# Kernel tuning notes

Hardware: AMD Instinct MI355X
Metric: run time of the kernel (lower is better)

## Reference

```python
import jax, jax.numpy as jnp
import numpy as np

N, E, B, F_IN, C, K = 200000, 3200000, 128, 128, 10, 30
D_CAT = 97  # 32+32+32+1 concatenated GCN outputs


def setup_inputs() -> dict:
    key = jax.random.key(0)
    ks = jax.random.split(key, 12)
    s = 0.1
    return {
        "x": jax.random.normal(ks[0], (N, F_IN), jnp.float32),
        "edge_index": jax.random.randint(ks[1], (2, E), 0, N, jnp.int32),
        "batch": jnp.sort(jax.random.randint(ks[2], (N,), 0, B, jnp.int32)),
        "W1": jax.random.normal(ks[3], (F_IN, 32), jnp.float32) * s,
        "b1": jnp.zeros((32,), jnp.float32),
        "W2": jax.random.normal(ks[4], (32, 32), jnp.float32) * s,
        "b2": jnp.zeros((32,), jnp.float32),
        "W3": jax.random.normal(ks[5], (32, 32), jnp.float32) * s,
        "b3": jnp.zeros((32,), jnp.float32),
        "W4": jax.random.normal(ks[6], (32, 1), jnp.float32) * s,
        "b4": jnp.zeros((1,), jnp.float32),
        "conv5_w": jax.random.normal(ks[7], (16, 1, 97), jnp.float32) * s,
        "conv5_b": jnp.zeros((16,), jnp.float32),
        "conv6_w": jax.random.normal(ks[8], (32, 16, 5), jnp.float32) * s,
        "conv6_b": jnp.zeros((32,), jnp.float32),
        "fc1_w": jax.random.normal(ks[9], (352, 128), jnp.float32) * s,
        "fc1_b": jnp.zeros((128,), jnp.float32),
        "fc2_w": jax.random.normal(ks[10], (128, C), jnp.float32) * s,
        "fc2_b": jnp.zeros((C,), jnp.float32),
    }


def _gcn(x, W, b, src, dst, enorm, self_norm):
    # PyG GCNConv: h = xW; out = sum_j norm_ij * h_j (incl. self loop) + b
    h = x @ W
    agg = jax.ops.segment_sum(h[src] * enorm[:, None], dst, num_segments=h.shape[0])
    return agg + h * self_norm[:, None] + b


def _conv1d(x, w, b, stride):
    y = jax.lax.conv_general_dilated(x, w, (stride,), 'VALID',
                                     dimension_numbers=('NCH', 'OIH', 'NCH'))
    return y + b[None, :, None]


def reference(x, edge_index, batch, W1, b1, W2, b2, W3, b3, W4, b4,
              conv5_w, conv5_b, conv6_w, conv6_b, fc1_w, fc1_b, fc2_w, fc2_b):
    src, dst = edge_index[0], edge_index[1]
    # remove_self_loops (zero edge weight) then GCN adds self loop of weight 1
    w = (src != dst).astype(x.dtype)
    deg = jax.ops.segment_sum(w, dst, num_segments=N) + 1.0
    dinv = jax.lax.rsqrt(deg)
    enorm = w * dinv[src] * dinv[dst]   # per-edge sym norm
    self_norm = 1.0 / deg               # self-loop norm = dinv[i]^2

    x1 = jnp.tanh(_gcn(x, W1, b1, src, dst, enorm, self_norm))
    x2 = jnp.tanh(_gcn(x1, W2, b2, src, dst, enorm, self_norm))
    x3 = jnp.tanh(_gcn(x2, W3, b3, src, dst, enorm, self_norm))
    x4 = jnp.tanh(_gcn(x3, W4, b4, src, dst, enorm, self_norm))
    xc = jnp.concatenate([x1, x2, x3, x4], axis=-1)  # [N, 97]

    # SortAggregation(k=30): per-graph top-k nodes by last channel (descending)
    keyf = xc[:, -1]
    graph_ids = jnp.arange(B, dtype=batch.dtype)
    scores = jnp.where(batch[None, :] == graph_ids[:, None], keyf[None, :],
                       jnp.float32(-jnp.inf))         # [B, N]
    topv, topi = jax.lax.top_k(scores, K)              # [B, K]
    feats = xc[topi]                                   # [B, K, 97]
    feats = jnp.where(jnp.isfinite(topv)[..., None], feats, 0.0)  # pad rows -> 0
    z = feats.reshape(B, 1, K * D_CAT)                 # [B, 1, 2910]

    z = jax.nn.relu(_conv1d(z, conv5_w, conv5_b, 97))  # [B, 16, 30]
    z = jax.lax.reduce_window(z, -jnp.inf, jax.lax.max,
                              (1, 1, 2), (1, 1, 2), 'VALID')  # [B, 16, 15]
    z = jax.nn.relu(_conv1d(z, conv6_w, conv6_b, 1))   # [B, 32, 11]
    z = z.reshape(B, -1)                               # [B, 352]
    h = jax.nn.relu(z @ fc1_w + fc1_b)                 # dropout = identity (eval)
    return jax.nn.log_softmax(h @ fc2_w + fc2_b, axis=-1)
```

## Files before the change

### kernel.cpp

```cpp
#include <hip/hip_runtime.h>
#include <math.h>

#define TPB 256
#define TOPK 30
#define NGRAPH 128
#define TKCAP 4096
#define BSHIFT 11
#define NBMAX 128
#define FSHIFT 8
#define NFMAX 800
#define FCAP 4608


__global__ void bhist(const int* __restrict__ src, const int* __restrict__ dst,
                      int* __restrict__ btot, int E) {
    __shared__ int bcnt[NBMAX];
    int t = threadIdx.x;
    int base = blockIdx.x * 2048;
    int lim = E - base; if (lim > 2048) lim = 2048;
    for (int i = t; i < NBMAX; i += 256) bcnt[i] = 0;
    __syncthreads();
    for (int i = t; i < lim; i += 256) {
        int s = src[base + i], d = dst[base + i];
        if (s != d) atomicAdd(&bcnt[d >> BSHIFT], 1);
    }
    __syncthreads();
    for (int i = t; i < NBMAX; i += 256)
        if (bcnt[i] > 0) atomicAdd(&btot[i], bcnt[i]);
}

__global__ void bucket_scan(const int* __restrict__ btot, int* __restrict__ bbase,
                            int nbuckets) {
    __shared__ int ls[NBMAX];
    int t = threadIdx.x;
    int v = (t < nbuckets) ? btot[t] : 0;
    ls[t] = v;
    __syncthreads();
    for (int o = 1; o < NBMAX; o <<= 1) {
        int x = 0;
        if (t >= o) x = ls[t - o];
        __syncthreads();
        ls[t] += x;
        __syncthreads();
    }
    if (t < nbuckets) bbase[t] = ls[t] - v;
}

__global__ void bin_edges(const int* __restrict__ src, const int* __restrict__ dst,
                          const int* __restrict__ bbase_g, int* __restrict__ gcur,
                          int2* __restrict__ scratch, int E) {
    __shared__ int2 eds[2048];
    __shared__ int bcnt[NBMAX], bbase[NBMAX], boff[NBMAX];
    int t = threadIdx.x;
    int base = blockIdx.x * 2048;
    int lim = E - base; if (lim > 2048) lim = 2048;
    for (int i = t; i < NBMAX; i += 256) { bcnt[i] = 0; boff[i] = 0; }
    __syncthreads();
    for (int i = t; i < lim; i += 256) {
        int s = src[base + i], d = dst[base + i];
        if (s == d) d = -1;
        eds[i] = make_int2(s, d);
        if (d >= 0) atomicAdd(&bcnt[d >> BSHIFT], 1);
    }
    __syncthreads();
    for (int i = t; i < NBMAX; i += 256) {
        if (bcnt[i] > 0)
            bbase[i] = bbase_g[i] + atomicAdd(&gcur[i], bcnt[i]);
    }
    __syncthreads();
    for (int i = t; i < lim; i += 256) {
        int2 ed = eds[i];
        if (ed.y >= 0) {
            int b = ed.y >> BSHIFT;
            int pos = bbase[b] + atomicAdd(&boff[b], 1);
            scratch[pos] = ed;
        }
    }
}

__global__ void bucket_count(const int2* __restrict__ scratch,
                             const int* __restrict__ bbase, const int* __restrict__ btot,
                             int* __restrict__ rowptr, float* __restrict__ dinv,
                             float* __restrict__ snorm, int N, int NB) {
    __shared__ int hist[1 << BSHIFT];
    __shared__ int ls2[256];
    int b = blockIdx.x, t = threadIdx.x;
    int nlo = b << BSHIFT;
    int nn = N - nlo; if (nn > (1 << BSHIFT)) nn = 1 << BSHIFT;
    for (int i = t; i < (1 << BSHIFT); i += 256) hist[i] = 0;
    __syncthreads();
    int lo = bbase[b], hi = lo + btot[b];
    for (int e = lo + t; e < hi; e += 256)
        atomicAdd(&hist[scratch[e].y - nlo], 1);
    __syncthreads();
    int loc[8]; int run = 0;
    #pragma unroll
    for (int j = 0; j < 8; ++j) { loc[j] = run; run += hist[t * 8 + j]; }
    ls2[t] = run;
    __syncthreads();
    for (int o = 1; o < 256; o <<= 1) {
        int x = (t >= o) ? ls2[t - o] : 0;
        __syncthreads();
        ls2[t] += x;
        __syncthreads();
    }
    int base = bbase[b] + ls2[t] - run;
    #pragma unroll
    for (int j = 0; j < 8; ++j) {
        int i = t * 8 + j;
        if (i < nn) {
            rowptr[nlo + i] = base + loc[j];
            int c = hist[i];
            float deg = (float)c + 1.0f;
            dinv[nlo + i] = 1.0f / sqrtf(deg);
            snorm[nlo + i] = 1.0f / deg;
        }
    }
    if (b == NB - 1 && t == 0) rowptr[N] = bbase[b] + btot[b];
}

__global__ void bin2(const int2* __restrict__ scratch, const int* __restrict__ rowptr,
                     int* __restrict__ fcur, int2* __restrict__ scratch2, int N, int E) {
    __shared__ int fcnt[NFMAX], fbase[NFMAX], foff[NFMAX];
    int t = threadIdx.x;
    int En = rowptr[N];
    int base = blockIdx.x * 8192;
    if (base >= En) return;
    int lim = En - base; if (lim > 8192) lim = 8192;
    for (int i = t; i < NFMAX; i += 256) { fcnt[i] = 0; foff[i] = 0; }
    __syncthreads();
    for (int i = t; i < lim; i += 256) {
        int d = scratch[base + i].y;
        atomicAdd(&fcnt[d >> FSHIFT], 1);
    }
    __syncthreads();
    for (int fi = t; fi < NFMAX; fi += 256) {
        if (fcnt[fi] > 0)
            fbase[fi] = rowptr[fi << FSHIFT] + atomicAdd(&fcur[fi], fcnt[fi]);
    }
    __syncthreads();
    for (int i = t; i < lim; i += 256) {
        int2 ed = scratch[base + i];
        int fi = ed.y >> FSHIFT;
        int pos = fbase[fi] + atomicAdd(&foff[fi], 1);
        scratch2[pos] = ed;
    }
}

__global__ __launch_bounds__(256) void scatter_sort(const int2* __restrict__ scratch2,
                                                    const int* __restrict__ rowptr,
                                                    const float* __restrict__ dinv,
                                                    int2* __restrict__ eprec, int N) {
    __shared__ int srcA[FCAP], dstA[FCAP], inv[FCAP];
    __shared__ int hist[1 << FSHIFT];
    __shared__ int hcur[1 << FSHIFT];
    int f = blockIdx.x, t = threadIdx.x;
    int nlo = f << FSHIFT;
    int nhi = nlo + (1 << FSHIFT); if (nhi > N) nhi = N;
    int lo = rowptr[nlo], hi = rowptr[nhi];
    int span = hi - lo;
    for (int i = t; i < (1 << FSHIFT); i += 256) hist[i] = 0;
    __syncthreads();
    if (span <= FCAP) {
        for (int i = t; i < span; i += 256) {
            int2 ed = scratch2[lo + i];
            srcA[i] = ed.x; dstA[i] = ed.y;
            atomicAdd(&hist[ed.y - nlo], 1);
        }
        __syncthreads();
        int v = hist[t];
        hcur[t] = v;
        __syncthreads();
        for (int o = 1; o < 256; o <<= 1) {
            int x = (t >= o) ? hcur[t - o] : 0;
            __syncthreads();
            hcur[t] += x;
            __syncthreads();
        }
        int excl = hcur[t] - v;
        __syncthreads();
        hcur[t] = excl;
        __syncthreads();
        for (int i = t; i < span; i += 256) {
            int slot = atomicAdd(&hcur[dstA[i] - nlo], 1);
            inv[slot] = i;
        }
        __syncthreads();
        for (int p = t; p < span; p += 256) {
            int i = inv[p];
            int s = srcA[i], d = dstA[i];
            eprec[lo + p] = make_int2(s, __float_as_int(dinv[s] * dinv[d]));
        }
    } else {
        for (int e = lo + t; e < hi; e += 256) {
            int2 ed = scratch2[e];
            int d = ed.y;
            int p = rowptr[d] + atomicAdd(&hist[d - nlo], 1);
            eprec[p] = make_int2(ed.x, __float_as_int(dinv[ed.x] * dinv[d]));
        }
    }
}


__global__ void mm_128_32(const float* __restrict__ X, const float* __restrict__ W,
                          float* __restrict__ H, int n) {
    __shared__ float Ws[128 * 32];
    __shared__ float xs[32 * 128];
    int t = threadIdx.x;
    int rbase = blockIdx.x * 32;
    #pragma unroll
    for (int j = 0; j < 4; ++j) {
        int idx = t + 256 * j;
        *(float4*)(Ws + idx * 4) = *(const float4*)(W + idx * 4);
        int row = rbase + (idx >> 5);
        float4 v = make_float4(0.f, 0.f, 0.f, 0.f);
        if (row < n) v = *(const float4*)(X + (long)rbase * 128 + idx * 4);
        *(float4*)(xs + idx * 4) = v;
    }
    __syncthreads();
    int c4 = (t & 7) * 4, r = t >> 3;
    int row = rbase + r;
    if (row >= n) return;
    float ac0 = 0.f, ac1 = 0.f, ac2 = 0.f, ac3 = 0.f;
    #pragma unroll 8
    for (int k0 = 0; k0 < 128; k0 += 4) {
        float4 xv = *(const float4*)(xs + r * 128 + k0);
        #pragma unroll
        for (int j = 0; j < 4; ++j) {
            float xj = (j == 0) ? xv.x : (j == 1) ? xv.y : (j == 2) ? xv.z : xv.w;
            float4 wv = *(const float4*)(Ws + (k0 + j) * 32 + c4);
            ac0 += xj * wv.x; ac1 += xj * wv.y; ac2 += xj * wv.z; ac3 += xj * wv.w;
        }
    }
    *(float4*)(H + (long)row * 32 + c4) = make_float4(ac0, ac1, ac2, ac3);
}

__global__ void mm_32_32(const float* __restrict__ X, const float* __restrict__ W,
                         float* __restrict__ H, int n) {
    __shared__ float Ws[32 * 32];
    __shared__ float xs[32 * 32];
    int t = threadIdx.x;
    int rbase = blockIdx.x * 32;
    {
        *(float4*)(Ws + t * 4) = *(const float4*)(W + t * 4);
        int row = rbase + (t >> 3);
        float4 v = make_float4(0.f, 0.f, 0.f, 0.f);
        if (row < n) v = *(const float4*)(X + (long)rbase * 32 + t * 4);
        *(float4*)(xs + t * 4) = v;
    }
    __syncthreads();
    int c4 = (t & 7) * 4, r = t >> 3;
    int row = rbase + r;
    if (row >= n) return;
    float ac0 = 0.f, ac1 = 0.f, ac2 = 0.f, ac3 = 0.f;
    #pragma unroll
    for (int k0 = 0; k0 < 32; k0 += 4) {
        float4 xv = *(const float4*)(xs + r * 32 + k0);
        #pragma unroll
        for (int j = 0; j < 4; ++j) {
            float xj = (j == 0) ? xv.x : (j == 1) ? xv.y : (j == 2) ? xv.z : xv.w;
            float4 wv = *(const float4*)(Ws + (k0 + j) * 32 + c4);
            ac0 += xj * wv.x; ac1 += xj * wv.y; ac2 += xj * wv.z; ac3 += xj * wv.w;
        }
    }
    *(float4*)(H + (long)row * 32 + c4) = make_float4(ac0, ac1, ac2, ac3);
}

__global__ void mm_32_1(const float* __restrict__ X, const float* __restrict__ W,
                        float* __restrict__ H4, int n) {
    int gid = blockIdx.x * blockDim.x + threadIdx.x;
    int node = gid >> 3, l = gid & 7;
    if (node >= n) return;
    float4 v = *(const float4*)(X + (long)node * 32 + l * 4);
    float s = v.x * W[l * 4] + v.y * W[l * 4 + 1] + v.z * W[l * 4 + 2] + v.w * W[l * 4 + 3];
    s += __shfl_xor(s, 1, 64);
    s += __shfl_xor(s, 2, 64);
    s += __shfl_xor(s, 4, 64);
    if (l == 0) H4[node] = s;
}


__global__ void agg32(const float* __restrict__ H, const int2* __restrict__ eprec,
                      const int* __restrict__ rowptr,
                      const float* __restrict__ snorm, const float* __restrict__ bias,
                      float* __restrict__ OUT, int n) {
    int gid = blockIdx.x * blockDim.x + threadIdx.x;
    int node = gid >> 3, l = gid & 7;
    if (node >= n) return;
    int beg = rowptr[node], end = rowptr[node + 1];
    float ax = 0.f, ay = 0.f, az = 0.f, aw = 0.f;
    int e0 = beg;
    for (; e0 + 8 <= end; e0 += 8) {
        int2 ed = eprec[e0 + l];
        int ss[8]; float ww[8];
        #pragma unroll
        for (int j = 0; j < 8; ++j) {
            ss[j] = __shfl(ed.x, j, 8);
            ww[j] = __shfl(__int_as_float(ed.y), j, 8);
        }
        float4 hv[8];
        #pragma unroll
        for (int j = 0; j < 8; ++j)
            hv[j] = *(const float4*)(H + (long)ss[j] * 32 + l * 4);
        #pragma unroll
        for (int j = 0; j < 8; ++j) {
            ax += hv[j].x * ww[j]; ay += hv[j].y * ww[j];
            az += hv[j].z * ww[j]; aw += hv[j].w * ww[j];
        }
    }
    if (e0 < end) {
        int m = end - e0;
        int2 ed = (l < m) ? eprec[e0 + l] : make_int2(0, 0);
        for (int j = 0; j < m; ++j) {
            int s = __shfl(ed.x, j, 8);
            float w = __shfl(__int_as_float(ed.y), j, 8);
            float4 hv = *(const float4*)(H + (long)s * 32 + l * 4);
            ax += hv.x * w; ay += hv.y * w; az += hv.z * w; aw += hv.w * w;
        }
    }
    float sn = snorm[node];
    float4 hv = *(const float4*)(H + (long)node * 32 + l * 4);
    float4 bv = *(const float4*)(bias + l * 4);
    float4 o;
    o.x = tanhf(ax + hv.x * sn + bv.x);
    o.y = tanhf(ay + hv.y * sn + bv.y);
    o.z = tanhf(az + hv.z * sn + bv.z);
    o.w = tanhf(aw + hv.w * sn + bv.w);
    *(float4*)(OUT + (long)node * 32 + l * 4) = o;
}

__global__ void agg1(const float* __restrict__ H4, const int2* __restrict__ eprec,
                     const int* __restrict__ rowptr,
                     const float* __restrict__ snorm, const float* __restrict__ b4,
                     float* __restrict__ X4, int n) {
    int node = blockIdx.x * blockDim.x + threadIdx.x;
    if (node >= n) return;
    int beg = rowptr[node], end = rowptr[node + 1];
    float acc = 0.f;
    for (int e = beg; e < end; ++e) {
        int2 ed = eprec[e];
        acc += H4[ed.x] * __int_as_float(ed.y);
    }
    X4[node] = tanhf(acc + H4[node] * snorm[node] + b4[0]);
}


__global__ void graph_start(const int* __restrict__ batch, int* __restrict__ gstart,
                            int n, int B) {
    int i = blockIdx.x * blockDim.x + threadIdx.x;
    if (i >= n) return;
    int b = batch[i];
    int bp = (i == 0) ? -1 : batch[i - 1];
    for (int g = bp + 1; g <= b; ++g) gstart[g] = i;
    if (i == n - 1) {
        for (int g = b + 1; g <= B; ++g) gstart[g] = n;
    }
}


__global__ __launch_bounds__(512) void topk_head(
        const float* __restrict__ x1, const float* __restrict__ x2,
        const float* __restrict__ x3, const float* __restrict__ x4,
        const int* __restrict__ gstart,
        const float* __restrict__ w5, const float* __restrict__ b5,
        const float* __restrict__ w6, const float* __restrict__ b6,
        const float* __restrict__ fw1, const float* __restrict__ fb1,
        const float* __restrict__ fw2, const float* __restrict__ fb2,
        float* __restrict__ out) {
    int g = blockIdx.x;
    int t = threadIdx.x;
    __shared__ int topi_l[TOPK];
    __shared__ int selg[TOPK];
    __shared__ float lv[4 * TOPK];
    __shared__ int li[4 * TOPK];
    __shared__ float vals[TKCAP];
    __shared__ float wbv[8];
    __shared__ int wbi[8];
    __shared__ float ws5[16 * 97];
    __shared__ float ws6[32 * 16 * 5];
    __shared__ float wf2[128 * 10];
    __shared__ float part[4][128];
    __shared__ float feats[TOPK][97];
    __shared__ float c5[16][30];
    __shared__ float p6[16][15];
    __shared__ float z[352];
    __shared__ float hh[128];
    __shared__ float oo[10];

    int beg = gstart[g], end = gstart[g + 1];
    int range = end - beg;

    if (range <= 2048) {
        if (t >= 256) {
            int u = t - 256;
            for (int i = u; i < 16 * 97; i += 256) ws5[i] = w5[i];
            for (int i = u; i < 32 * 16 * 5; i += 256) ws6[i] = w6[i];
            for (int i = u; i < 128 * 10; i += 256) wf2[i] = fw2[i];
        } else {
            int wv = t >> 6, l = t & 63;
            int chunk = (range + 3) >> 2;
            int cbeg = wv * chunk;
            int cend = cbeg + chunk; if (cend > range) cend = range;
            float rv[8];
            #pragma unroll
            for (int j = 0; j < 8; ++j) {
                int i = cbeg + l + (j << 6);
                rv[j] = (i < cend) ? x4[beg + i] : -INFINITY;
            }
            for (int k = 0; k < TOPK; ++k) {
                float best = -INFINITY;
                int bj = -1;
                #pragma unroll
                for (int j = 0; j < 8; ++j)
                    if (rv[j] > best) { best = rv[j]; bj = j; }
                int bi = (bj < 0) ? 0x7fffffff : cbeg + (bj << 6) + l;
                #pragma unroll
                for (int off = 1; off < 64; off <<= 1) {
                    float ov = __shfl_xor(best, off, 64);
                    int oi = __shfl_xor(bi, off, 64);
                    if (ov > best || (ov == best && oi < bi)) { best = ov; bi = oi; }
                }
                if (l == 0) { lv[wv * TOPK + k] = best; li[wv * TOPK + k] = bi; }
                if (bi != 0x7fffffff && ((bi - cbeg) & 63) == l) {
                    int wj = (bi - cbeg) >> 6;
                    #pragma unroll
                    for (int j = 0; j < 8; ++j)
                        if (j == wj) rv[j] = -INFINITY;
                }
            }
        }
        __syncthreads();
        if (t < 64) {
            float mv0 = lv[t];
            int   mi0 = li[t];
            int i1 = t + 64;
            float mv1 = (i1 < 120) ? lv[i1] : -INFINITY;
            int   mi1 = (i1 < 120) ? li[i1] : 0x7fffffff;
            for (int k = 0; k < TOPK; ++k) {
                float best = mv0; int bi = mi0;
                if (mv1 > best || (mv1 == best && mi1 < bi)) { best = mv1; bi = mi1; }
                #pragma unroll
                for (int off = 1; off < 64; off <<= 1) {
                    float ov = __shfl_xor(best, off, 64);
                    int oi = __shfl_xor(bi, off, 64);
                    if (ov > best || (ov == best && oi < bi)) { best = ov; bi = oi; }
                }
                if (t == 0)
                    topi_l[k] = (bi == 0x7fffffff) ? -1 : beg + bi;
                if (mi0 == bi) mv0 = -INFINITY;
                if (mi1 == bi) mv1 = -INFINITY;
            }
        }
    } else {
        if (t >= 256) {
            int u = t - 256;
            for (int i = u; i < 16 * 97; i += 256) ws5[i] = w5[i];
            for (int i = u; i < 32 * 16 * 5; i += 256) ws6[i] = w6[i];
            for (int i = u; i < 128 * 10; i += 256) wf2[i] = fw2[i];
        }
        int lim = range < TKCAP ? range : TKCAP;
        for (int i = t; i < lim; i += 512) vals[i] = x4[beg + i];
        __syncthreads();
        for (int k = 0; k < TOPK; ++k) {
            float best = -INFINITY;
            int bi = 0x7fffffff;
            for (int i = t; i < lim; i += 512) {
                float v = vals[i];
                if (v > best) { best = v; bi = i; }
            }
            for (int i = TKCAP + t; i < range; i += 512) {
                int gi = beg + i;
                bool taken = false;
                for (int j = 0; j < k; ++j)
                    if (selg[j] == gi) { taken = true; break; }
                if (taken) continue;
                float v = x4[gi];
                if (v > best || (v == best && i < bi)) { best = v; bi = i; }
            }
            #pragma unroll
            for (int off = 1; off < 64; off <<= 1) {
                float ov = __shfl_xor(best, off, 64);
                int oi = __shfl_xor(bi, off, 64);
                if (ov > best || (ov == best && oi < bi)) { best = ov; bi = oi; }
            }
            if ((t & 63) == 0) { wbv[t >> 6] = best; wbi[t >> 6] = bi; }
            __syncthreads();
            if (t == 0) {
                float bv = wbv[0]; int bi0 = wbi[0];
                for (int wq = 1; wq < 8; ++wq)
                    if (wbv[wq] > bv || (wbv[wq] == bv && wbi[wq] < bi0)) { bv = wbv[wq]; bi0 = wbi[wq]; }
                int gl = (bi0 == 0x7fffffff) ? -1 : beg + bi0;
                selg[k] = gl;
                topi_l[k] = gl;
                if (bi0 != 0x7fffffff && bi0 < TKCAP) vals[bi0] = -INFINITY;
            }
            __syncthreads();
        }
    }
    __syncthreads();

    for (int idx = t; idx < TOPK * 97; idx += 512) {
        int k = idx / 97, j = idx % 97;
        int node = topi_l[k];
        float v = 0.f;
        if (node >= 0) {
            if (j < 32) v = x1[(long)node * 32 + j];
            else if (j < 64) v = x2[(long)node * 32 + (j - 32)];
            else if (j < 96) v = x3[(long)node * 32 + (j - 64)];
            else v = x4[node];
        }
        feats[k][j] = v;
    }
    __syncthreads();

    for (int idx = t; idx < 16 * 30; idx += 512) {
        int oc = idx / 30, k = idx % 30;
        float acc = b5[oc];
        for (int j = 0; j < 97; ++j) acc += ws5[oc * 97 + j] * feats[k][j];
        c5[oc][k] = fmaxf(acc, 0.f);
    }
    __syncthreads();

    for (int idx = t; idx < 16 * 15; idx += 512) {
        int oc = idx / 15, k = idx % 15;
        p6[oc][k] = fmaxf(c5[oc][2 * k], c5[oc][2 * k + 1]);
    }
    __syncthreads();

    for (int idx = t; idx < 32 * 11; idx += 512) {
        int oc = idx / 11, tt = idx % 11;
        float acc = b6[oc];
        for (int ic = 0; ic < 16; ++ic)
            for (int j = 0; j < 5; ++j)
                acc += ws6[(oc * 16 + ic) * 5 + j] * p6[ic][tt + j];
        z[idx] = fmaxf(acc, 0.f);
    }
    __syncthreads();

    {
        int o = t & 127, s = t >> 7;
        float acc = 0.f;
        int i0 = s * 88, i1 = i0 + 88;
        for (int i = i0; i < i1; ++i) acc += z[i] * fw1[i * 128 + o];
        part[s][o] = acc;
    }
    __syncthreads();
    if (t < 128) {
        float v = fb1[t] + ((part[0][t] + part[1][t]) + (part[2][t] + part[3][t]));
        hh[t] = fmaxf(v, 0.f);
    }
    __syncthreads();

    if (t < 10) {
        float acc = fb2[t];
        for (int j = 0; j < 128; ++j) acc += hh[j] * wf2[j * 10 + t];
        oo[t] = acc;
    }
    __syncthreads();

    if (t < 10) {
        float m = -INFINITY;
        for (int c = 0; c < 10; ++c) m = fmaxf(m, oo[c]);
        float s = 0.f;
        for (int c = 0; c < 10; ++c) s += expf(oo[c] - m);
        out[g * 10 + t] = oo[t] - m - logf(s);
    }
}


extern "C" void kernel_launch(void* const* d_in, const int* in_sizes, int n_in,
                              void* d_out, int out_size, void* d_ws, size_t ws_size,
                              hipStream_t stream) {
    const float* x     = (const float*)d_in[0];
    const int*   ei    = (const int*)d_in[1];
    const int*   batch = (const int*)d_in[2];
    const float* W1 = (const float*)d_in[3];
    const float* b1 = (const float*)d_in[4];
    const float* W2 = (const float*)d_in[5];
    const float* b2 = (const float*)d_in[6];
    const float* W3 = (const float*)d_in[7];
    const float* b3 = (const float*)d_in[8];
    const float* W4 = (const float*)d_in[9];
    const float* b4 = (const float*)d_in[10];
    const float* w5 = (const float*)d_in[11];
    const float* b5 = (const float*)d_in[12];
    const float* w6 = (const float*)d_in[13];
    const float* b6 = (const float*)d_in[14];
    const float* fw1 = (const float*)d_in[15];
    const float* fb1 = (const float*)d_in[16];
    const float* fw2 = (const float*)d_in[17];
    const float* fb2 = (const float*)d_in[18];

    const int N = in_sizes[0] / 128;
    const int E = in_sizes[1] / 2;
    const int* src = ei;
    const int* dst = ei + E;

    char* w = (char*)d_ws;
    size_t off = 0;
    auto alloc = [&](size_t bytes) -> void* {
        void* p = w + off;
        off = (off + bytes + 255) & ~(size_t)255;
        return p;
    };

    int*   gcur   = (int*)alloc(NBMAX * 4);
    int*   btot   = (int*)alloc(NBMAX * 4);
    int*   fcur   = (int*)alloc(NFMAX * 4);
    int*   bbase  = (int*)alloc(NBMAX * 4);
    int*   gstart = (int*)alloc((size_t)(NGRAPH + 1) * 4);
    int*   rowptr = (int*)alloc((size_t)(N + 1) * 4);
    float* dinv   = (float*)alloc((size_t)N * 4);
    float* snorm  = (float*)alloc((size_t)N * 4);
    int2*  eprec  = (int2*)alloc((size_t)E * 8);
    float* hbuf   = (float*)alloc((size_t)N * 32 * 4);
    float* x1     = (float*)alloc((size_t)N * 32 * 4);
    float* x2     = (float*)alloc((size_t)N * 32 * 4);
    float* x3     = (float*)alloc((size_t)N * 32 * 4);
    float* h4     = (float*)alloc((size_t)N * 4);
    float* x4     = (float*)alloc((size_t)N * 4);

    int2* scratch  = (int2*)hbuf;
    int2* scratch2 = (int2*)x1;

    hipMemsetAsync(gcur, 0, (size_t)(2 * NBMAX + NFMAX) * 4, stream);

    const int NB = (N + (1 << BSHIFT) - 1) >> BSHIFT;
    const int NF = (N + (1 << FSHIFT) - 1) >> FSHIFT;
    const int EB = (E + 2047) / 2048;

    graph_start<<<(N + TPB - 1) / TPB, TPB, 0, stream>>>(batch, gstart, N, NGRAPH);
    bhist<<<EB, TPB, 0, stream>>>(src, dst, btot, E);
    bucket_scan<<<1, NBMAX, 0, stream>>>(btot, bbase, NB);
    bin_edges<<<EB, TPB, 0, stream>>>(src, dst, bbase, gcur, scratch, E);
    bucket_count<<<NB, TPB, 0, stream>>>(scratch, bbase, btot, rowptr, dinv, snorm, N, NB);
    bin2<<<(E + 8191) / 8192, TPB, 0, stream>>>(scratch, rowptr, fcur, scratch2, N, E);
    scatter_sort<<<NF, 256, 0, stream>>>(scratch2, rowptr, dinv, eprec, N);

    mm_128_32<<<(N + 31) / 32, 256, 0, stream>>>(x, W1, hbuf, N);
    agg32<<<((size_t)N * 8 + TPB - 1) / TPB, TPB, 0, stream>>>(hbuf, eprec, rowptr,
                                                               snorm, b1, x1, N);
    mm_32_32<<<(N + 31) / 32, 256, 0, stream>>>(x1, W2, hbuf, N);
    agg32<<<((size_t)N * 8 + TPB - 1) / TPB, TPB, 0, stream>>>(hbuf, eprec, rowptr,
                                                               snorm, b2, x2, N);
    mm_32_32<<<(N + 31) / 32, 256, 0, stream>>>(x2, W3, hbuf, N);
    agg32<<<((size_t)N * 8 + TPB - 1) / TPB, TPB, 0, stream>>>(hbuf, eprec, rowptr,
                                                               snorm, b3, x3, N);
    mm_32_1<<<((size_t)N * 8 + TPB - 1) / TPB, TPB, 0, stream>>>(x3, W4, h4, N);
    agg1<<<(N + TPB - 1) / TPB, TPB, 0, stream>>>(h4, eprec, rowptr, snorm, b4, x4, N);

    topk_head<<<NGRAPH, 512, 0, stream>>>(x1, x2, x3, x4, gstart,
                                          w5, b5, w6, b6, fw1, fb1, fw2, fb2,
                                          (float*)d_out);
}
```

Baseline: 554.5 us.

## Replace iterative top-k selection with per-wave bitonic sort and sorted merge

In the small-graph path of the top-k head kernel, all 8 waves now each load up to 256 keys and bitonic-sort them in registers with shuffles. Each wave writes its top 30, and a single wave then bitonic-sorts the 240 candidates to get the final top-k. This replaces 30 rounds of argmax-plus-shuffle reductions in 4 waves followed by a 30-round merge. Weight loading moves to the remaining 448 threads after the per-wave sort. The fixed bitonic network costs more shuffle steps per wave but has no serial loop over k, and it assumes each wave's chunk fits in 256 elements (range at most 2048).

```diff
diff --git a/kernel.cpp b/kernel.cpp
--- a/kernel.cpp
+++ b/kernel.cpp
@@ -358,6 +358,43 @@
 }
 
 
+#define GTP(av,ai,bv,bi) (((av) > (bv)) || ((av) == (bv) && (ai) < (bi)))
+
+__device__ __forceinline__ void bsort256(float& v0, float& v1, float& v2, float& v3,
+                                         int& i0, int& i1, int& i2, int& i3, int lane) {
+    for (int k = 2; k <= 256; k <<= 1) {
+        for (int j = k >> 1; j > 0; j >>= 1) {
+            if (j == 64) {
+                { bool down = ((lane) & k) == 0;
+                  bool agt = GTP(v0, i0, v1, i1);
+                  if (down != agt) { float tv = v0; v0 = v1; v1 = tv; int ti = i0; i0 = i1; i1 = ti; } }
+                { bool down = ((lane + 128) & k) == 0;
+                  bool agt = GTP(v2, i2, v3, i3);
+                  if (down != agt) { float tv = v2; v2 = v3; v3 = tv; int ti = i2; i2 = i3; i3 = ti; } }
+            } else if (j == 128) {
+                { bool down = ((lane) & k) == 0;
+                  bool agt = GTP(v0, i0, v2, i2);
+                  if (down != agt) { float tv = v0; v0 = v2; v2 = tv; int ti = i0; i0 = i2; i2 = ti; } }
+                { bool down = ((lane + 64) & k) == 0;
+                  bool agt = GTP(v1, i1, v3, i3);
+                  if (down != agt) { float tv = v1; v1 = v3; v3 = tv; int ti = i1; i1 = i3; i3 = ti; } }
+            } else {
+                #define XSTEP(vv, ii, ebase) { \
+                    float ov = __shfl_xor(vv, j, 64); \
+                    int   oi = __shfl_xor(ii, j, 64); \
+                    bool down = ((lane + (ebase)) & k) == 0; \
+                    bool low  = (lane & j) == 0; \
+                    bool win  = GTP(vv, ii, ov, oi); \
+                    bool keep = (down == low) ? win : !win; \
+                    if (!keep) { vv = ov; ii = oi; } }
+                XSTEP(v0, i0, 0) XSTEP(v1, i1, 64) XSTEP(v2, i2, 128) XSTEP(v3, i3, 192)
+                #undef XSTEP
+            }
+        }
+    }
+}
+
+
 __global__ __launch_bounds__(512) void topk_head(
         const float* __restrict__ x1, const float* __restrict__ x2,
         const float* __restrict__ x3, const float* __restrict__ x4,
@@ -371,8 +408,8 @@
     int t = threadIdx.x;
     __shared__ int topi_l[TOPK];
     __shared__ int selg[TOPK];
-    __shared__ float lv[4 * TOPK];
-    __shared__ int li[4 * TOPK];
+    __shared__ float lv[8 * TOPK];
+    __shared__ int li[8 * TOPK];
     __shared__ float vals[TKCAP];
     __shared__ float wbv[8];
     __shared__ int wbi[8];
@@ -391,65 +428,47 @@
     int range = end - beg;
 
     if (range <= 2048) {
-        if (t >= 256) {
-            int u = t - 256;
-            for (int i = u; i < 16 * 97; i += 256) ws5[i] = w5[i];
-            for (int i = u; i < 32 * 16 * 5; i += 256) ws6[i] = w6[i];
-            for (int i = u; i < 128 * 10; i += 256) wf2[i] = fw2[i];
+        int wv = t >> 6, lane = t & 63;
+        int csz = (range + 7) >> 3;
+        int cbeg = wv * csz;
+        float v0, v1, v2, v3; int j0, j1, j2, j3;
+        {
+            int id0 = lane, id1 = lane + 64, id2 = lane + 128, id3 = lane + 192;
+            bool k0 = (id0 < csz) && (cbeg + id0 < range);
+            bool k1 = (id1 < csz) && (cbeg + id1 < range);
+            bool k2 = (id2 < csz) && (cbeg + id2 < range);
+            bool k3 = (id3 < csz) && (cbeg + id3 < range);
+            v0 = k0 ? x4[beg + cbeg + id0] : -INFINITY;
+            v1 = k1 ? x4[beg + cbeg + id1] : -INFINITY;
+            v2 = k2 ? x4[beg + cbeg + id2] : -INFINITY;
+            v3 = k3 ? x4[beg + cbeg + id3] : -INFINITY;
+            j0 = k0 ? (cbeg + id0) : (0x0FFFF000 + id0);
+            j1 = k1 ? (cbeg + id1) : (0x0FFFF000 + id1);
+            j2 = k2 ? (cbeg + id2) : (0x0FFFF000 + id2);
+            j3 = k3 ? (cbeg + id3) : (0x0FFFF000 + id3);
+        }
+        bsort256(v0, v1, v2, v3, j0, j1, j2, j3, lane);
+        if (lane < TOPK) { lv[wv * TOPK + lane] = v0; li[wv * TOPK + lane] = j0; }
+        __syncthreads();
+        if (t < 64) {
+            float m0, m1, m2, m3; int n0, n1, n2, n3;
+            int id0 = t, id1 = t + 64, id2 = t + 128, id3 = t + 192;
+            m0 = (id0 < 8 * TOPK) ? lv[id0] : -INFINITY;
+            m1 = (id1 < 8 * TOPK) ? lv[id1] : -INFINITY;
+            m2 = (id2 < 8 * TOPK) ? lv[id2] : -INFINITY;
+            m3 = (id3 < 8 * TOPK) ? lv[id3] : -INFINITY;
+            n0 = (id0 < 8 * TOPK) ? li[id0] : (0x0FFFF000 + id0);
+            n1 = (id1 < 8 * TOPK) ? li[id1] : (0x0FFFF000 + id1);
+            n2 = (id2 < 8 * TOPK) ? li[id2] : (0x0FFFF000 + id2);
+            n3 = (id3 < 8 * TOPK) ? li[id3] : (0x0FFFF000 + id3);
+            bsort256(m0, m1, m2, m3, n0, n1, n2, n3, t);
+            if (t < TOPK)
+                topi_l[t] = (m0 == -INFINITY) ? -1 : beg + n0;
         } else {
-            int wv = t >> 6, l = t & 63;
-            int chunk = (range + 3) >> 2;
-            int cbeg = wv * chunk;
-            int cend = cbeg + chunk; if (cend > range) cend = range;
-            float rv[8];
-            #pragma unroll
-            for (int j = 0; j < 8; ++j) {
-                int i = cbeg + l + (j << 6);
-                rv[j] = (i < cend) ? x4[beg + i] : -INFINITY;
-            }
-            for (int k = 0; k < TOPK; ++k) {
-                float best = -INFINITY;
-                int bj = -1;
-                #pragma unroll
-                for (int j = 0; j < 8; ++j)
-                    if (rv[j] > best) { best = rv[j]; bj = j; }
-                int bi = (bj < 0) ? 0x7fffffff : cbeg + (bj << 6) + l;
-                #pragma unroll
-                for (int off = 1; off < 64; off <<= 1) {
-                    float ov = __shfl_xor(best, off, 64);
-                    int oi = __shfl_xor(bi, off, 64);
-                    if (ov > best || (ov == best && oi < bi)) { best = ov; bi = oi; }
-                }
-                if (l == 0) { lv[wv * TOPK + k] = best; li[wv * TOPK + k] = bi; }
-                if (bi != 0x7fffffff && ((bi - cbeg) & 63) == l) {
-                    int wj = (bi - cbeg) >> 6;
-                    #pragma unroll
-                    for (int j = 0; j < 8; ++j)
-                        if (j == wj) rv[j] = -INFINITY;
-                }
-            }
-        }
-        __syncthreads();
-        if (t < 64) {
-            float mv0 = lv[t];
-            int   mi0 = li[t];
-            int i1 = t + 64;
-            float mv1 = (i1 < 120) ? lv[i1] : -INFINITY;
-            int   mi1 = (i1 < 120) ? li[i1] : 0x7fffffff;
-            for (int k = 0; k < TOPK; ++k) {
-                float best = mv0; int bi = mi0;
-                if (mv1 > best || (mv1 == best && mi1 < bi)) { best = mv1; bi = mi1; }
-                #pragma unroll
-                for (int off = 1; off < 64; off <<= 1) {
-                    float ov = __shfl_xor(best, off, 64);
-                    int oi = __shfl_xor(bi, off, 64);
-                    if (ov > best || (ov == best && oi < bi)) { best = ov; bi = oi; }
-                }
-                if (t == 0)
-                    topi_l[k] = (bi == 0x7fffffff) ? -1 : beg + bi;
-                if (mi0 == bi) mv0 = -INFINITY;
-                if (mi1 == bi) mv1 = -INFINITY;
-            }
+            int u = t - 64;
+            for (int i = u; i < 16 * 97; i += 448) ws5[i] = w5[i];
+            for (int i = u; i < 32 * 16 * 5; i += 448) ws6[i] = w6[i];
+            for (int i = u; i < 128 * 10; i += 448) wf2[i] = fw2[i];
         }
     } else {
         if (t >= 256) {
```

Result: no change. 549.1 us (-1.0%).
